# Performance work log

Measured on AMD Instinct MI355X. Metric: run time of the kernel, lower is better.

The kernel has to match this reference:

```python
import jax, jax.numpy as jnp
import numpy as np
import math

N_FILT = 80
FILT_DIM = 251
FS = 16000
MIN_FREQ = 50.0
MIN_BAND = 50.0


def _init_params():
    low_freq_mel = 80.0
    high_freq_mel = 2595.0 * np.log10(1.0 + FS / 2.0 / 700.0)
    mel_points = np.linspace(low_freq_mel, high_freq_mel, N_FILT)
    f_cos = 700.0 * (10.0 ** (mel_points / 2595.0) - 1.0)
    b1 = np.roll(f_cos, 1)
    b2 = np.roll(f_cos, -1)
    b1[0] = 30.0
    b2[-1] = FS / 2.0 - 100.0
    freq_scale = FS * 1.0
    return (jnp.asarray(b1 / freq_scale, dtype=jnp.float32),
            jnp.asarray((b2 - b1) / freq_scale, dtype=jnp.float32))


def setup_inputs() -> dict:
    key = jax.random.key(0)
    x = jax.random.normal(key, (32, 1, 32000), dtype=jnp.float32)
    filt_b1, filt_band = _init_params()
    return {"x": x, "filt_b1": filt_b1, "filt_band": filt_band}


def _sinc_batch(band, t_right):
    # band: [F] (in Hz, already scaled by fs); t_right: [T] (seconds)
    arg = 2.0 * math.pi * band[:, None] * t_right[None, :]  # [F, T]
    y_right = jnp.sin(arg) / arg
    y_left = y_right[:, ::-1]
    ones = jnp.ones((band.shape[0], 1), dtype=band.dtype)
    return jnp.concatenate([y_left, ones, y_right], axis=1)  # [F, 2T+1]


def _build_filters(filt_b1, filt_band):
    N = FILT_DIM
    freq_scale = float(FS)
    t_right = (jnp.linspace(1.0, (N - 1) / 2.0, (N - 1) // 2) / FS).astype(jnp.float32)
    filt_beg = jnp.abs(filt_b1) + MIN_FREQ / freq_scale            # [F]
    filt_end = filt_beg + (jnp.abs(filt_band) + MIN_BAND / freq_scale)
    # torch.linspace(0, N, steps=N): N points from 0 to N inclusive
    n = jnp.linspace(0.0, float(N), N).astype(jnp.float32)
    window = (0.54 - 0.46 * jnp.cos(2.0 * math.pi * n / N)).astype(jnp.float32)
    low_pass1 = 2.0 * filt_beg[:, None] * _sinc_batch(filt_beg * freq_scale, t_right)
    low_pass2 = 2.0 * filt_end[:, None] * _sinc_batch(filt_end * freq_scale, t_right)
    band_pass = low_pass2 - low_pass1                              # [F, N]
    band_pass = band_pass / jnp.max(band_pass, axis=1, keepdims=True)
    return band_pass * window[None, :]                             # [F, N]


def reference(x, filt_b1, filt_band):
    filters = _build_filters(filt_b1, filt_band)                   # [N_filt, Filt_dim]
    out = jax.lax.conv_general_dilated(
        x, filters[:, None, :],
        window_strides=(1,), padding='VALID',
        dimension_numbers=('NCH', 'OIH', 'NCH'))
    return out  # [B, N_filt, L - Filt_dim + 1]
```

## Files before the change

### kernel.cpp

```cpp
#include <hip/hip_runtime.h>
#include <math.h>

#define N_FILT   80
#define FILT_DIM 251
#define KPAD     256
#define SIG_LEN  32000
#define OUT_LEN  31750
#define BATCH    32
#define TPB      256

#define STRIP    1024
#define WAVE_T   256
#define NREP     8
#define LROW     644
#define OBSTRIDE 66

#define TWO_PI_F 6.28318530717958647692f

typedef __attribute__((ext_vector_type(8))) short    short8;
typedef __attribute__((ext_vector_type(8))) _Float16 half8;
typedef __attribute__((ext_vector_type(4))) float    float4v;

__global__ __launch_bounds__(TPB) void build_filters_kernel(
    const float* __restrict__ b1, const float* __restrict__ band,
    unsigned short* __restrict__ fh)
{
    const int f = blockIdx.x;
    const int i = threadIdx.x;

    const float MINF = 50.0f / 16000.0f;
    const float fb = fabsf(b1[f]) + MINF;
    const float fe = fb + fabsf(band[f]) + MINF;

    float v = 0.0f;
    if (i < FILT_DIM) {
        int m = i - 125; m = (m < 0) ? -m : m;
        if (m == 0) v = 2.0f * fe - 2.0f * fb;
        else {
            float a1 = TWO_PI_F * fb * (float)m;
            float a2 = TWO_PI_F * fe * (float)m;
            v = 2.0f * fe * (sinf(a2) / a2) - 2.0f * fb * (sinf(a1) / a1);
        }
    }

    __shared__ float red[TPB];
    red[i] = (i < FILT_DIM) ? v : -INFINITY;
    __syncthreads();
    #pragma unroll
    for (int s = TPB / 2; s > 0; s >>= 1) {
        if (i < s) red[i] = fmaxf(red[i], red[i + s]);
        __syncthreads();
    }
    const float mx = red[0];

    const float w   = 0.54f - 0.46f * cosf(TWO_PI_F * (float)i / 250.0f);
    const float val = (i < FILT_DIM) ? (v / mx) * w : 0.0f;
    const _Float16 h = (_Float16)val;
    fh[f * KPAD + i] = __builtin_bit_cast(unsigned short, h);
}

__global__ __launch_bounds__(TPB, 4) void sinc_mfma_kernel(
    const float* __restrict__ x,
    const unsigned short* __restrict__ fh,
    float* __restrict__ out)
{
    __shared__ __align__(16) unsigned xf[NREP * LROW];
    __shared__ __align__(16) float    ob[4][16 * OBSTRIDE];

    const int tid   = threadIdx.x;
    const int strip = blockIdx.x;
    const int fb    = blockIdx.y;
    const int n     = blockIdx.z;
    const int e0    = strip * STRIP;
    const float* xp = x + (size_t)n * SIG_LEN;

    for (int d = tid; d < LROW; d += TPB) {
        const int g = e0 + 2 * d;
        float v0, v1, v2;
        if (g + 2 < SIG_LEN) {
            float2 p = *(const float2*)(xp + g);
            v0 = p.x; v1 = p.y; v2 = xp[g + 2];
        } else {
            v0 = (g     < SIG_LEN) ? xp[g]     : 0.0f;
            v1 = (g + 1 < SIG_LEN) ? xp[g + 1] : 0.0f;
            v2 = (g + 2 < SIG_LEN) ? xp[g + 2] : 0.0f;
        }
        const _Float16 h0 = (_Float16)v0, h1 = (_Float16)v1, h2 = (_Float16)v2;
        union { _Float16 h[2]; unsigned u; } pe, po;
        pe.h[0] = h0; pe.h[1] = h1;
        po.h[0] = h1; po.h[1] = h2;
        xf[0 * LROW + d] = pe.u;
        xf[1 * LROW + d] = po.u;
        if (d >= 1) { xf[2 * LROW + d - 1] = pe.u;
                      xf[3 * LROW + d - 1] = po.u; }
        if (d >= 2) { xf[4 * LROW + d - 2] = pe.u;
                      xf[5 * LROW + d - 2] = po.u; }
        if (d >= 3) { xf[6 * LROW + d - 3] = pe.u;
                      xf[7 * LROW + d - 3] = po.u; }
    }

    const int lane = tid & 63;
    const int w    = tid >> 6;
    const int m    = lane & 15;
    const int q    = lane >> 4;
    short8 Ah[8];
    {
        const unsigned short* ph = fh + (fb * 16 + m) * KPAD + q * 8;
        #pragma unroll
        for (int kb = 0; kb < 8; ++kb)
            Ah[kb] = *(const short8*)(ph + kb * 32);
    }
    __syncthreads();

    const int r = m & 7;
    const unsigned base = (unsigned)(r * LROW + 4 * (m >> 3) + 4 * q + 128 * w);

    float* const obw = &ob[w][0];
    const int    c2    = 2 * (lane & 31);
    const int    rhalf = lane >> 5;
    const size_t rowb  = ((size_t)n * N_FILT + fb * 16) * OUT_LEN;

    for (int g = 0; g < 4; ++g) {
        #pragma unroll
        for (int tl = 0; tl < 4; ++tl) {
            const int tt = g * 4 + tl;
            float4v a0 = {0.f,0.f,0.f,0.f}, a1 = {0.f,0.f,0.f,0.f};
            const unsigned o0 = base + 8 * tt;
            #pragma unroll
            for (int kk = 0; kk < 4; ++kk) {
                a0 = __builtin_amdgcn_mfma_f32_16x16x32_f16(
                         __builtin_bit_cast(half8, Ah[2*kk]),
                         __builtin_bit_cast(half8, *(const uint4*)(&xf[o0 + 32*kk])),
                         a0, 0, 0, 0);
                a1 = __builtin_amdgcn_mfma_f32_16x16x32_f16(
                         __builtin_bit_cast(half8, Ah[2*kk+1]),
                         __builtin_bit_cast(half8, *(const uint4*)(&xf[o0 + 32*kk + 16])),
                         a1, 0, 0, 0);
            }
            const int oc = tl * 16 + m;
            #pragma unroll
            for (int rg = 0; rg < 4; ++rg)
                obw[(q * 4 + rg) * OBSTRIDE + oc] = a0[rg] + a1[rg];
        }

        const int t = e0 + w * WAVE_T + g * 64 + c2;
        if (t + 1 < OUT_LEN) {
            #pragma unroll
            for (int f = 0; f < 8; ++f) {
                const int rr = 2 * f + rhalf;
                const float2 v = *(const float2*)(&obw[rr * OBSTRIDE + c2]);
                *(float2*)(out + rowb + (size_t)rr * OUT_LEN + t) = v;
            }
        }
    }
}

extern "C" void kernel_launch(void* const* d_in, const int* in_sizes, int n_in,
                              void* d_out, int out_size, void* d_ws, size_t ws_size,
                              hipStream_t stream)
{
    const float* x    = (const float*)d_in[0];
    const float* b1   = (const float*)d_in[1];
    const float* band = (const float*)d_in[2];
    float* outp = (float*)d_out;

    unsigned short* fh = (unsigned short*)d_ws;

    build_filters_kernel<<<dim3(N_FILT), dim3(TPB), 0, stream>>>(b1, band, fh);

    dim3 grid((OUT_LEN + STRIP - 1) / STRIP, N_FILT / 16, BATCH);
    sinc_mfma_kernel<<<grid, dim3(TPB), 0, stream>>>(x, fh, outp);
}
```

Before: 105.2 us.

## Interleave wave time tiles and stage output through shared block buffer

Remaps MFMA tiles so the four waves work on interleaved 16-column tiles within 512-output halves instead of contiguous 256-output quarters. Results go into one shared 16x516 buffer, and each wave then writes 4 full filter rows of 512 contiguous floats. This should give longer coalesced global stores per row, and the tail now writes single elements when an odd column is left over. The cost is two block-wide barriers per half, the looser launch bounds that drop the occupancy hint, and a larger shared output buffer.

```diff
diff --git a/kernel.cpp b/kernel.cpp
--- a/kernel.cpp
+++ b/kernel.cpp
@@ -10,10 +10,9 @@
 #define TPB      256
 
 #define STRIP    1024
-#define WAVE_T   256
 #define NREP     8
 #define LROW     644
-#define OBSTRIDE 66
+#define OBS      516
 
 #define TWO_PI_F 6.28318530717958647692f
 
@@ -59,13 +58,13 @@
     fh[f * KPAD + i] = __builtin_bit_cast(unsigned short, h);
 }
 
-__global__ __launch_bounds__(TPB, 4) void sinc_mfma_kernel(
+__global__ __launch_bounds__(TPB) void sinc_mfma_kernel(
     const float* __restrict__ x,
     const unsigned short* __restrict__ fh,
     float* __restrict__ out)
 {
     __shared__ __align__(16) unsigned xf[NREP * LROW];
-    __shared__ __align__(16) float    ob[4][16 * OBSTRIDE];
+    __shared__ __align__(16) float    ob[16 * OBS];
 
     const int tid   = threadIdx.x;
     const int strip = blockIdx.x;
@@ -113,19 +112,16 @@
     __syncthreads();
 
     const int r = m & 7;
-    const unsigned base = (unsigned)(r * LROW + 4 * (m >> 3) + 4 * q + 128 * w);
+    const unsigned base = (unsigned)(r * LROW + 8 * w + 4 * (m >> 3) + 4 * q);
 
-    float* const obw = &ob[w][0];
-    const int    c2    = 2 * (lane & 31);
-    const int    rhalf = lane >> 5;
-    const size_t rowb  = ((size_t)n * N_FILT + fb * 16) * OUT_LEN;
+    const size_t outrow0 = ((size_t)n * N_FILT + fb * 16) * OUT_LEN;
 
-    for (int g = 0; g < 4; ++g) {
+    for (int p = 0; p < 2; ++p) {
         #pragma unroll
-        for (int tl = 0; tl < 4; ++tl) {
-            const int tt = g * 4 + tl;
+        for (int tg = 0; tg < 8; ++tg) {
+            const int tt = p * 8 + tg;
             float4v a0 = {0.f,0.f,0.f,0.f}, a1 = {0.f,0.f,0.f,0.f};
-            const unsigned o0 = base + 8 * tt;
+            const unsigned o0 = base + 32u * tt;
             #pragma unroll
             for (int kk = 0; kk < 4; ++kk) {
                 a0 = __builtin_amdgcn_mfma_f32_16x16x32_f16(
@@ -137,21 +133,30 @@
                          __builtin_bit_cast(half8, *(const uint4*)(&xf[o0 + 32*kk + 16])),
                          a1, 0, 0, 0);
             }
-            const int oc = tl * 16 + m;
+            const int oc = tg * 64 + w * 16 + m;
             #pragma unroll
             for (int rg = 0; rg < 4; ++rg)
-                obw[(q * 4 + rg) * OBSTRIDE + oc] = a0[rg] + a1[rg];
+                ob[(q * 4 + rg) * OBS + oc] = a0[rg] + a1[rg];
         }
+        __syncthreads();
 
-        const int t = e0 + w * WAVE_T + g * 64 + c2;
-        if (t + 1 < OUT_LEN) {
+        #pragma unroll
+        for (int j = 0; j < 4; ++j) {
+            const int row = 4 * w + j;
+            float* const dst = out + outrow0 + (size_t)row * OUT_LEN;
             #pragma unroll
-            for (int f = 0; f < 8; ++f) {
-                const int rr = 2 * f + rhalf;
-                const float2 v = *(const float2*)(&obw[rr * OBSTRIDE + c2]);
-                *(float2*)(out + rowb + (size_t)rr * OUT_LEN + t) = v;
+            for (int h = 0; h < 4; ++h) {
+                const int c  = h * 128 + 2 * lane;
+                const int t0 = e0 + p * 512 + c;
+                if (t0 + 1 < OUT_LEN) {
+                    const float2 v = *(const float2*)(&ob[row * OBS + c]);
+                    *(float2*)(dst + t0) = v;
+                } else if (t0 < OUT_LEN) {
+                    dst[t0] = ob[row * OBS + c];
+                }
             }
         }
+        __syncthreads();
     }
 }
 
```

After: 102.1 us. 1.03x faster.

## Cover all 80 filters per block with five waves, swizzle block index

Applied to the files above, without the earlier changes.

Each block now runs five waves, one per 16-filter group, over the full 1024-sample strip. Before, there were five filter-group blocks per strip, and each one converted and staged the same input in LDS. The change removes that redundant global load and fp16 conversion of x. A swizzled 1D grid maps blocks to (strip, batch). Each wave now does four times more MFMA tiles serially, and the grid has a fifth as many blocks, which changes occupancy and latency hiding.

```diff
diff --git a/kernel.cpp b/kernel.cpp
--- a/kernel.cpp
+++ b/kernel.cpp
@@ -7,13 +7,13 @@
 #define SIG_LEN  32000
 #define OUT_LEN  31750
 #define BATCH    32
-#define TPB      256
+#define TPB      320
 
 #define STRIP    1024
-#define WAVE_T   256
 #define NREP     8
 #define LROW     644
-#define OBSTRIDE 66
+#define OBS      80
+#define NTILE    64
 
 #define TWO_PI_F 6.28318530717958647692f
 
@@ -21,7 +21,7 @@
 typedef __attribute__((ext_vector_type(8))) _Float16 half8;
 typedef __attribute__((ext_vector_type(4))) float    float4v;
 
-__global__ __launch_bounds__(TPB) void build_filters_kernel(
+__global__ __launch_bounds__(256) void build_filters_kernel(
     const float* __restrict__ b1, const float* __restrict__ band,
     unsigned short* __restrict__ fh)
 {
@@ -43,11 +43,11 @@
         }
     }
 
-    __shared__ float red[TPB];
+    __shared__ float red[256];
     red[i] = (i < FILT_DIM) ? v : -INFINITY;
     __syncthreads();
     #pragma unroll
-    for (int s = TPB / 2; s > 0; s >>= 1) {
+    for (int s = 128; s > 0; s >>= 1) {
         if (i < s) red[i] = fmaxf(red[i], red[i + s]);
         __syncthreads();
     }
@@ -65,12 +65,13 @@
     float* __restrict__ out)
 {
     __shared__ __align__(16) unsigned xf[NREP * LROW];
-    __shared__ __align__(16) float    ob[4][16 * OBSTRIDE];
+    __shared__ __align__(16) float    ob[5][16 * OBS];
 
-    const int tid   = threadIdx.x;
-    const int strip = blockIdx.x;
-    const int fb    = blockIdx.y;
-    const int n     = blockIdx.z;
+    const int tid = threadIdx.x;
+    const unsigned raw = blockIdx.x;
+    const unsigned swz = (raw & 7u) * 128u + (raw >> 3);
+    const int strip = (int)(swz & 31u);
+    const int n     = (int)(swz >> 5);
     const int e0    = strip * STRIP;
     const float* xp = x + (size_t)n * SIG_LEN;
 
@@ -105,7 +106,7 @@
     const int q    = lane >> 4;
     short8 Ah[8];
     {
-        const unsigned short* ph = fh + (fb * 16 + m) * KPAD + q * 8;
+        const unsigned short* ph = fh + (w * 16 + m) * KPAD + q * 8;
         #pragma unroll
         for (int kb = 0; kb < 8; ++kb)
             Ah[kb] = *(const short8*)(ph + kb * 32);
@@ -113,19 +114,19 @@
     __syncthreads();
 
     const int r = m & 7;
-    const unsigned base = (unsigned)(r * LROW + 4 * (m >> 3) + 4 * q + 128 * w);
+    const unsigned base = (unsigned)(r * LROW + 4 * (m >> 3) + 4 * q);
 
-    float* const obw = &ob[w][0];
-    const int    c2    = 2 * (lane & 31);
-    const int    rhalf = lane >> 5;
-    const size_t rowb  = ((size_t)n * N_FILT + fb * 16) * OUT_LEN;
+    float* const obw  = &ob[w][0];
+    const int    c2   = 2 * (lane & 31);
+    const int    rh   = lane >> 5;
+    const size_t row0 = ((size_t)n * N_FILT + w * 16) * OUT_LEN;
 
-    for (int g = 0; g < 4; ++g) {
+    for (int g = 0; g < 16; ++g) {
         #pragma unroll
         for (int tl = 0; tl < 4; ++tl) {
             const int tt = g * 4 + tl;
             float4v a0 = {0.f,0.f,0.f,0.f}, a1 = {0.f,0.f,0.f,0.f};
-            const unsigned o0 = base + 8 * tt;
+            const unsigned o0 = base + 8u * tt;
             #pragma unroll
             for (int kk = 0; kk < 4; ++kk) {
                 a0 = __builtin_amdgcn_mfma_f32_16x16x32_f16(
@@ -140,16 +141,16 @@
             const int oc = tl * 16 + m;
             #pragma unroll
             for (int rg = 0; rg < 4; ++rg)
-                obw[(q * 4 + rg) * OBSTRIDE + oc] = a0[rg] + a1[rg];
+                obw[(q * 4 + rg) * OBS + oc] = a0[rg] + a1[rg];
         }
 
-        const int t = e0 + w * WAVE_T + g * 64 + c2;
-        if (t + 1 < OUT_LEN) {
+        const int t0 = e0 + g * 64 + c2;
+        if (t0 + 1 < OUT_LEN) {
             #pragma unroll
             for (int f = 0; f < 8; ++f) {
-                const int rr = 2 * f + rhalf;
-                const float2 v = *(const float2*)(&obw[rr * OBSTRIDE + c2]);
-                *(float2*)(out + rowb + (size_t)rr * OUT_LEN + t) = v;
+                const int row = 2 * f + rh;
+                const float2 v = *(const float2*)(&obw[row * OBS + c2]);
+                *(float2*)(out + row0 + (size_t)row * OUT_LEN + t0) = v;
             }
         }
     }
@@ -166,8 +167,8 @@
 
     unsigned short* fh = (unsigned short*)d_ws;
 
-    build_filters_kernel<<<dim3(N_FILT), dim3(TPB), 0, stream>>>(b1, band, fh);
+    build_filters_kernel<<<dim3(N_FILT), dim3(256), 0, stream>>>(b1, band, fh);
 
-    dim3 grid((OUT_LEN + STRIP - 1) / STRIP, N_FILT / 16, BATCH);
+    dim3 grid(32 * 32);
     sinc_mfma_kernel<<<grid, dim3(TPB), 0, stream>>>(x, fh, outp);
 }
```

New measurement: 93.22 us. 1.13x faster.
